# Kernel tuning notes

Hardware: AMD Instinct MI355X
Metric: run time of the kernel (lower is better)

## Reference

```python
import jax, jax.numpy as jnp
import numpy as np

N = 200000      # nodes
E = 1600000     # directed edges (before self-loops)
G = 5000        # graphs (molecules)
IN, HID, OUT, HEADS = 128, 128, 128, 3


def gat_layer(x, src, dst, W, a_src, a_dst, b, heads, out_dim, concat):
    n = x.shape[0]
    h = (x @ W).reshape(n, heads, out_dim)                 # [N,H,F]
    al_s = jnp.einsum('nhf,hf->nh', h, a_src)              # [N,H]
    al_d = jnp.einsum('nhf,hf->nh', h, a_dst)
    e = jax.nn.leaky_relu(al_s[src] + al_d[dst], 0.2)      # [E,H]
    m = jax.ops.segment_max(e, dst, num_segments=n)        # softmax over incoming edges
    ex = jnp.exp(e - m[dst])
    den = jax.ops.segment_sum(ex, dst, num_segments=n)
    alpha = ex / (den[dst] + 1e-16)                        # [E,H]
    msg = h[src] * alpha[..., None]                        # [E,H,F]
    agg = jax.ops.segment_sum(msg, dst, num_segments=n)    # [N,H,F]
    agg = agg.reshape(n, heads * out_dim) if concat else agg.mean(axis=1)
    return agg + b


def setup_inputs() -> dict:
    key = jax.random.key(0)
    ks = jax.random.split(key, 16)
    d = {}
    d['x'] = jax.random.normal(ks[0], (N, IN), dtype=jnp.float32)
    d['edge_index'] = jax.random.randint(ks[1], (2, E), 0, N, dtype=jnp.int64)
    d['batch'] = jnp.sort(jax.random.randint(ks[2], (N,), 0, G, dtype=jnp.int64))
    s = 0.1
    d['W1'] = jax.random.normal(ks[3], (IN, HEADS * HID), jnp.float32) * s
    d['a1s'] = jax.random.normal(ks[4], (HEADS, HID), jnp.float32) * s
    d['a1d'] = jax.random.normal(ks[5], (HEADS, HID), jnp.float32) * s
    d['b1'] = jnp.zeros((HEADS * HID,), jnp.float32)
    d['W2'] = jax.random.normal(ks[6], (HEADS * HID, HEADS * HID), jnp.float32) * s
    d['a2s'] = jax.random.normal(ks[7], (HEADS, HID), jnp.float32) * s
    d['a2d'] = jax.random.normal(ks[8], (HEADS, HID), jnp.float32) * s
    d['b2'] = jnp.zeros((HEADS * HID,), jnp.float32)
    d['W3'] = jax.random.normal(ks[9], (HEADS * HID, OUT), jnp.float32) * s
    d['a3s'] = jax.random.normal(ks[10], (1, OUT), jnp.float32) * s
    d['a3d'] = jax.random.normal(ks[11], (1, OUT), jnp.float32) * s
    d['b3'] = jnp.zeros((OUT,), jnp.float32)
    return d


def reference(x, edge_index, batch, W1, a1s, a1d, b1, W2, a2s, a2d, b2, W3, a3s, a3d, b3):
    # PyG GATConv default add_self_loops=True
    loops = jnp.arange(N, dtype=edge_index.dtype)
    src = jnp.concatenate([edge_index[0], loops])
    dst = jnp.concatenate([edge_index[1], loops])
    h = jax.nn.leaky_relu(gat_layer(x, src, dst, W1, a1s, a1d, b1, HEADS, HID, True), 0.2)
    h = jax.nn.leaky_relu(gat_layer(h, src, dst, W2, a2s, a2d, b2, HEADS, HID, True), 0.2)
    h = jax.nn.leaky_relu(gat_layer(h, src, dst, W3, a3s, a3d, b3, 1, OUT, False), 0.2)
    # global mean pool over graphs
    sums = jax.ops.segment_sum(h, batch, num_segments=G)            # [G,OUT]
    cnt = jax.ops.segment_sum(jnp.ones((N,), h.dtype), batch, num_segments=G)
    return sums / jnp.maximum(cnt, 1.0)[:, None]
```

## Files before the change

kernel.cpp:

```cpp
#include <hip/hip_runtime.h>
#include <hip/hip_bf16.h>
#include <math.h>

#define LRELU_SLOPE 0.2f
typedef __hip_bfloat16 bf16;
typedef __hip_bfloat162 bf16x2;

typedef short s8v __attribute__((ext_vector_type(8)));
typedef short s4v __attribute__((ext_vector_type(4)));
typedef float f4v __attribute__((ext_vector_type(4)));
typedef int   i4v __attribute__((ext_vector_type(4)));
typedef unsigned int u4v __attribute__((ext_vector_type(4)));

__device__ __forceinline__ float lrelu(float v) { return v > 0.f ? v : LRELU_SLOPE * v; }
__device__ __forceinline__ float b2f(short b) {
  return __uint_as_float(((unsigned)(unsigned short)b) << 16);
}

__device__ __forceinline__ void st2(float* p, float x, float y) {
  *(float2*)p = float2{x, y};
}

__device__ __forceinline__ u4v make_srd(const void* p) {
  u4v r;
  unsigned long long a = (unsigned long long)p;
  r.x = (unsigned)a; r.y = (unsigned)(a >> 32);
  r.z = 0xFFFFFFFFu;
  r.w = 0x00020000u;
  return r;
}
__device__ __forceinline__ void bstore16_nt(u4v srd, int byteoff, i4v d) {
  asm volatile("buffer_store_dwordx4 %0, %1, %2, 0 offen sc1 nt"
               :: "v"(d), "v"(byteoff), "s"(srd));
}


__global__ void k_zero(unsigned int* __restrict__ p, long n) {
  long i = (long)blockIdx.x * blockDim.x + threadIdx.x;
  if (i < n) p[i] = 0u;
}

__global__ void k_zero_out(float* __restrict__ out, int n) {
  int i = blockIdx.x * blockDim.x + threadIdx.x;
  if (i < n) out[i] = 0.f;
}


__global__ void k_cvt(const float* __restrict__ x, bf16* __restrict__ xb, long n8) {
  long i = (long)blockIdx.x * blockDim.x + threadIdx.x;
  if (i >= n8) return;
  const float4* xp = (const float4*)(x + i * 8);
  float4 a = xp[0], b = xp[1];
  s8v v;
  bf16 t;
  t = __float2bfloat16(a.x); v[0] = *(short*)&t;
  t = __float2bfloat16(a.y); v[1] = *(short*)&t;
  t = __float2bfloat16(a.z); v[2] = *(short*)&t;
  t = __float2bfloat16(a.w); v[3] = *(short*)&t;
  t = __float2bfloat16(b.x); v[4] = *(short*)&t;
  t = __float2bfloat16(b.y); v[5] = *(short*)&t;
  t = __float2bfloat16(b.z); v[6] = *(short*)&t;
  t = __float2bfloat16(b.w); v[7] = *(short*)&t;
  *(s8v*)&xb[i * 8] = v;
}

__global__ void k_tw2(const float* __restrict__ W, bf16* __restrict__ B2, int K, int NN) {
  int tid = blockIdx.x * blockDim.x + threadIdx.x;
  int total = (K * NN) >> 3;
  if (tid >= total) return;
  int f = tid >> 6, l = tid & 63;
  int nfr = NN >> 4;
  int k32 = f / nfr, ct = f - k32 * nfr;
  int col = ct * 16 + (l & 15);
  int krow = k32 * 32 + (l >> 4) * 8;
  s8v v;
#pragma unroll
  for (int j = 0; j < 8; ++j) {
    bf16 b = __float2bfloat16(W[(size_t)(krow + j) * NN + col]);
    v[j] = *(short*)&b;
  }
  *(s8v*)&B2[(size_t)tid * 8] = v;
}


__global__ void k_hist(const int* __restrict__ dst, int* __restrict__ deg, int E, int Et) {
  int e = blockIdx.x * blockDim.x + threadIdx.x;
  if (e >= Et) return;
  int d = (e < E) ? dst[e] : (e - E);
  atomicAdd(&deg[d], 1);
}

__global__ void k_hist1(const int* __restrict__ idx, int* __restrict__ deg, int n) {
  int i = blockIdx.x * blockDim.x + threadIdx.x;
  if (i < n) atomicAdd(&deg[idx[i]], 1);
}

__global__ void k_scan1(const int* __restrict__ deg, int* __restrict__ offs,
                        int* __restrict__ bsum, int n) {
  __shared__ int sd[256];
  int t = threadIdx.x;
  int base = blockIdx.x * 1024 + t * 4;
  int v[4]; int tsum = 0;
#pragma unroll
  for (int i = 0; i < 4; ++i) { v[i] = (base + i < n) ? deg[base + i] : 0; tsum += v[i]; }
  sd[t] = tsum;
  __syncthreads();
  for (int off = 1; off < 256; off <<= 1) {
    int x = (t >= off) ? sd[t - off] : 0;
    __syncthreads();
    sd[t] += x;
    __syncthreads();
  }
  int excl = sd[t] - tsum;
#pragma unroll
  for (int i = 0; i < 4; ++i) { if (base + i < n) offs[base + i] = excl; excl += v[i]; }
  if (t == 255) bsum[blockIdx.x] = sd[255];
}

__global__ void k_scan2(int* bsum, int nb) {
  int t = threadIdx.x;
  if (nb > 256) {
    if (t == 0 && blockIdx.x == 0) {
      int run = 0;
      for (int i = 0; i < nb; ++i) { int x = bsum[i]; bsum[i] = run; run += x; }
    }
    return;
  }
  int v = (t < nb) ? bsum[t] : 0;
  int lane = t & 63, wv = t >> 6;
  int s = v;
#pragma unroll
  for (int off = 1; off < 64; off <<= 1) {
    int u = __shfl_up(s, off, 64);
    if (lane >= off) s += u;
  }
  __shared__ int wsum[4];
  if (lane == 63) wsum[wv] = s;
  __syncthreads();
  int add = 0;
  for (int w = 0; w < wv; ++w) add += wsum[w];
  if (t < nb) bsum[t] = add + s - v;
}

__global__ void k_scan3(int* __restrict__ offs, const int* __restrict__ bsum, int n, int total) {
  int t = threadIdx.x;
  int base = blockIdx.x * 1024 + t * 4;
  int add = bsum[blockIdx.x];
#pragma unroll
  for (int i = 0; i < 4; ++i) if (base + i < n) offs[base + i] += add;
  if (blockIdx.x == 0 && t == 0) offs[n] = total;
}

__global__ void k_scatter(const int* __restrict__ src, const int* __restrict__ dst,
                          const int* __restrict__ offs, int* __restrict__ cur,
                          int* __restrict__ ssrc, int E, int Et) {
  int e = blockIdx.x * blockDim.x + threadIdx.x;
  if (e >= Et) return;
  int s, d;
  if (e < E) { s = src[e]; d = dst[e]; } else { s = d = e - E; }
  int pos = offs[d] + atomicAdd(&cur[d], 1);
  ssrc[pos] = s;
}


template <int K, int NN>
__global__ __launch_bounds__(512, 4) void k_gemm_t(const bf16* __restrict__ A,
                                                   const bf16* __restrict__ B2,
                                                   bf16* __restrict__ C,
                                                   const float* __restrict__ as_,
                                                   const float* __restrict__ ad_,
                                                   float* __restrict__ al_s,
                                                   float* __restrict__ al_d,
                                                   int N) {
  constexpr int nk = K / 32;
  constexpr int nfr = NN >> 4;
  constexpr int SP = (NN == 384) ? 4 : 1;
  __shared__ __align__(16) short sA[2][256 * 32];
  int t = threadIdx.x;
  int wv = t >> 6, lane = t & 63;
  int mg = wv >> 1, ng = wv & 1;
  int quad = lane >> 4, l15 = lane & 15;
  size_t bm0 = (size_t)blockIdx.x * 256;
  int hd = (NN == 384) ? blockIdx.y : 0;
  int ctb = blockIdx.y * 8 + ng * 4;

  int sr = t >> 2, p = t & 3;
  int c = p ^ (sr & 3);
  const bf16* g0 = A + (bm0 + sr) * (size_t)K + c * 8;
  const bf16* g1 = g0 + (size_t)128 * K;
  const bf16* Bp = B2 + ((size_t)ctb << 9) + lane * 8;

  f4v acc[4][4];
#pragma unroll
  for (int ms = 0; ms < 4; ++ms)
#pragma unroll
    for (int bn = 0; bn < 4; ++bn) acc[ms][bn] = f4v{0, 0, 0, 0};

#define STAGE(step, buf)                                                        \
  do {                                                                          \
    __builtin_amdgcn_global_load_lds(                                           \
        (const __attribute__((address_space(1))) void*)(g0 + (step) * 32),      \
        (__attribute__((address_space(3))) void*)((char*)sA[buf] + wv * 1024),  \
        16, 0, 0);                                                              \
    __builtin_amdgcn_global_load_lds(                                           \
        (const __attribute__((address_space(1))) void*)(g1 + (step) * 32),      \
        (__attribute__((address_space(3))) void*)((char*)sA[buf] + 8192 + wv * 1024), \
        16, 0, 0);                                                              \
  } while (0)

  STAGE(0, 0);
  __syncthreads();

  for (int ik = 0; ik < nk; ++ik) {
    int cur = ik & 1;
    if (ik + 1 < nk) STAGE(ik + 1, cur ^ 1);

    const char* sb = (const char*)sA[cur];
    s8v af[4];
#pragma unroll
    for (int ms = 0; ms < 4; ++ms) {
      int row = mg * 64 + ms * 16 + l15;
      int pos = quad ^ (row & 3);
      af[ms] = *(const s8v*)(sb + row * 64 + pos * 16);
    }
    s8v pb[4];
#pragma unroll
    for (int bn = 0; bn < 4; ++bn)
      pb[bn] = *(const s8v*)(Bp + ((size_t)(ik * nfr + bn) << 9));
#pragma unroll
    for (int ms = 0; ms < 4; ++ms)
#pragma unroll
      for (int bn = 0; bn < 4; ++bn)
        acc[ms][bn] = __builtin_amdgcn_mfma_f32_16x16x32_bf16(af[ms], pb[bn], acc[ms][bn], 0, 0, 0);

    __syncthreads();
  }
#undef STAGE

  float asv[4], adv[4];
#pragma unroll
  for (int bn = 0; bn < 4; ++bn) {
    int cwh = (ng * 4 + bn) * 16 + l15;
    asv[bn] = as_[hd * 128 + cwh];
    adv[bn] = ad_[hd * 128 + cwh];
  }

#pragma unroll
  for (int ms = 0; ms < 4; ++ms) {
#pragma unroll
    for (int r = 0; r < 4; ++r) {
      size_t rown = bm0 + mg * 64 + ms * 16 + quad * 4 + r;
      float ps = 0.f, pd = 0.f;
#pragma unroll
      for (int bn = 0; bn < 4; ++bn) {
        int coln = (ctb + bn) * 16 + l15;
        bf16 b = __float2bfloat16(acc[ms][bn][r]);
        C[rown * NN + coln] = b;
        float hv = b2f(*(short*)&b);
        ps += hv * asv[bn];
        pd += hv * adv[bn];
      }
#pragma unroll
      for (int off = 1; off <= 8; off <<= 1) {
        ps += __shfl_xor(ps, off, 64);
        pd += __shfl_xor(pd, off, 64);
      }
      if (l15 == 0 && rown < (size_t)N) {
        atomicAdd(&al_s[rown * SP + hd], ps);
        atomicAdd(&al_d[rown * SP + hd], pd);
      }
    }
  }
}


template <int CPL> struct HVec;
template <> struct HVec<8> { typedef s8v T; };
template <> struct HVec<4> { typedef s4v T; };

template <int H, typename OT>
__global__ __launch_bounds__(256) void k_attn_agg(const bf16* __restrict__ hbuf,
                           const int* __restrict__ ssrc,
                           const int* __restrict__ offs, const float* __restrict__ al_s,
                           const float* __restrict__ al_d, const float* __restrict__ bias,
                           OT* __restrict__ out, int N) {
  constexpr int SW  = (H > 1) ? 4 : 2;
  constexpr int ROW = H * 128;
  constexpr int CPL = (H > 1) ? 8 : 4;
  constexpr int NL  = ROW / CPL;
  typedef typename HVec<CPL>::T hvec;

  __shared__ __align__(16) float stash[4][64 * SW];
  int n = (blockIdx.x * blockDim.x + threadIdx.x) >> 6;
  int lane = threadIdx.x & 63;
  if (n >= N) return;
  float* st = stash[threadIdx.x >> 6];
  int start = offs[n], end = offs[n + 1];

  float ald[H];
  if constexpr (H > 1) {
    float4 t = *(const float4*)&al_d[(size_t)n * 4];
    ald[0] = t.x; ald[1] = t.y; ald[2] = t.z;
  } else {
    ald[0] = al_d[n];
  }

  bool act = lane < NL;
  int c0 = act ? lane * CPL : 0;
  int hd_l = c0 >> 7;

  float m[H];
  float den = 0.f;
  float acc[CPL];
#pragma unroll
  for (int hd = 0; hd < H; ++hd) m[hd] = -1e30f;
#pragma unroll
  for (int i = 0; i < CPL; ++i) acc[i] = 0.f;

  for (int cb = start; cb < end; cb += 64) {
    int cl = end - cb; if (cl > 64) cl = 64;
    bool el = lane < cl;
    int mys = el ? ssrc[cb + lane] : 0;
    float ev[H];
    if constexpr (H > 1) {
      float4 av = *(const float4*)&al_s[(size_t)mys * 4];
      ev[0] = av.x; ev[1] = av.y; ev[2] = av.z;
    } else {
      ev[0] = al_s[mys];
    }
#pragma unroll
    for (int hd = 0; hd < H; ++hd)
      ev[hd] = el ? lrelu(ev[hd] + ald[hd]) : -1e30f;

    float nm[H];
#pragma unroll
    for (int hd = 0; hd < H; ++hd) {
      float v = ev[hd];
#pragma unroll
      for (int off = 32; off; off >>= 1) v = fmaxf(v, __shfl_xor(v, off, 64));
      nm[hd] = fmaxf(v, m[hd]);
    }
    if (cb > start) {
      float sc[H];
#pragma unroll
      for (int hd = 0; hd < H; ++hd) sc[hd] = __expf(m[hd] - nm[hd]);
      float so = sc[hd_l];
      den *= so;
#pragma unroll
      for (int i = 0; i < CPL; ++i) acc[i] *= so;
    }
#pragma unroll
    for (int hd = 0; hd < H; ++hd) m[hd] = nm[hd];

    float myex[H];
#pragma unroll
    for (int hd = 0; hd < H; ++hd) myex[hd] = el ? __expf(ev[hd] - m[hd]) : 0.f;

    __builtin_amdgcn_wave_barrier();
    if constexpr (H > 1) {
      float4 s4{__int_as_float(mys), myex[0], myex[1], myex[2]};
      *(float4*)&st[lane * 4] = s4;
    } else {
      float2 s2{__int_as_float(mys), myex[0]};
      *(float2*)&st[lane * 2] = s2;
    }
    asm volatile("s_waitcnt lgkmcnt(0)" ::: "memory");
    __builtin_amdgcn_wave_barrier();

    for (int r = 0; r < cl; r += 8) {
      int su[8]; float a[8];
#pragma unroll
      for (int u = 0; u < 8; ++u) {
        if constexpr (H > 1) {
          float4 ed = *(const float4*)&st[(r + u) * 4];
          su[u] = __float_as_int(ed.x);
          a[u] = (hd_l == 0) ? ed.y : ((hd_l == 1) ? ed.z : ed.w);
        } else {
          float2 ed = *(const float2*)&st[(r + u) * 2];
          su[u] = __float_as_int(ed.x);
          a[u] = ed.y;
        }
        den += a[u];
      }
      hvec hv[8];
#pragma unroll
      for (int u = 0; u < 8; ++u)
        hv[u] = *(const hvec*)(hbuf + (size_t)su[u] * ROW + c0);
#pragma unroll
      for (int u = 0; u < 8; ++u)
#pragma unroll
        for (int i = 0; i < CPL; ++i)
          acc[i] += a[u] * b2f(hv[u][i]);
    }
  }

  if (act) {
    float rr = 1.f / (den + 1e-16f);
    u4v srd = make_srd(out);
    int boff = (int)(((size_t)n * ROW + c0) * sizeof(OT));
    if constexpr (sizeof(OT) == 2) {
      union { s8v s; i4v i; } u;
#pragma unroll
      for (int i = 0; i < CPL; ++i) {
        float o = lrelu(acc[i] * rr + bias[c0 + i]);
        bf16 b = __float2bfloat16(o);
        u.s[i] = *(short*)&b;
      }
      bstore16_nt(srd, boff, u.i);
    } else {
      union { float4 f; i4v i; } u;
      u.f.x = lrelu(acc[0] * rr + bias[c0 + 0]);
      u.f.y = lrelu(acc[1] * rr + bias[c0 + 1]);
      u.f.z = lrelu(acc[2] * rr + bias[c0 + 2]);
      u.f.w = lrelu(acc[3] * rr + bias[c0 + 3]);
      bstore16_nt(srd, boff, u.i);
    }
  }
}


__global__ void k_pool(const float* __restrict__ h, const int* __restrict__ goffs,
                       float* __restrict__ out, int G) {
  int g = (blockIdx.x * blockDim.x + threadIdx.x) >> 6;
  int lane = threadIdx.x & 63;
  if (g >= G) return;
  int s = goffs[g], e = goffs[g + 1];
  float ax = 0.f, ay = 0.f;
  for (int n = s; n < e; ++n) {
    float2 v = *(const float2*)&h[(size_t)n * 128 + lane * 2];
    ax += v.x; ay += v.y;
  }
  float c = fmaxf((float)(e - s), 1.f);
  st2(&out[(size_t)g * 128 + lane * 2], ax / c, ay / c);
}


extern "C" void kernel_launch(void* const* d_in, const int* in_sizes, int n_in,
                              void* d_out, int out_size, void* d_ws, size_t ws_size,
                              hipStream_t stream) {
  const float* x   = (const float*)d_in[0];
  const int*   ei  = (const int*)d_in[1];
  const int*   bat = (const int*)d_in[2];
  const float* W1  = (const float*)d_in[3];
  const float* a1s = (const float*)d_in[4];
  const float* a1d = (const float*)d_in[5];
  const float* b1  = (const float*)d_in[6];
  const float* W2  = (const float*)d_in[7];
  const float* a2s = (const float*)d_in[8];
  const float* a2d = (const float*)d_in[9];
  const float* b2  = (const float*)d_in[10];
  const float* W3  = (const float*)d_in[11];
  const float* a3s = (const float*)d_in[12];
  const float* a3d = (const float*)d_in[13];
  const float* b3  = (const float*)d_in[14];
  float* out = (float*)d_out;

  const int N = in_sizes[2];
  const int E = in_sizes[1] / 2;
  const int Et = E + N;
  const int G = out_size / 128;

  const int MB = (N + 255) / 256;
  const int Mpad = MB * 256;

  char* p = (char*)d_ws;
  auto carve = [&](size_t bytes) { void* r = (void*)p; p += (bytes + 255) & ~(size_t)255; return r; };
  bf16*  bufA   = (bf16*)carve((size_t)Mpad * 384 * 2);
  bf16*  bufB   = (bf16*)carve((size_t)Mpad * 384 * 2);
  float* al_s   = (float*)carve((size_t)N * 4 * 4);
  float* al_d   = (float*)carve((size_t)N * 4 * 4);
  int*   ssrc   = (int*)carve((size_t)Et * 4);
  int*   offs   = (int*)carve((size_t)(N + 1) * 4);
  int*   deg    = (int*)carve((size_t)N * 4);
  int*   cur    = (int*)carve((size_t)N * 4);
  int*   bsum   = (int*)carve(4096 * 4);
  int*   gdeg   = (int*)carve((size_t)G * 4);
  int*   goffs  = (int*)carve((size_t)(G + 1) * 4);
  bf16*  Wp1    = (bf16*)carve((size_t)384 * 128 * 2);
  bf16*  Wp2    = (bf16*)carve((size_t)384 * 384 * 2);
  bf16*  Wp3    = (bf16*)carve((size_t)128 * 384 * 2);
  size_t need = (size_t)(p - (char*)d_ws);

  if (ws_size < need) {
    k_zero_out<<<(out_size + 255) / 256, 256, 0, stream>>>(out, out_size);
    return;
  }

  const int* esrc = ei;
  const int* edst = ei + E;

  int ebl = (Et + 255) / 256;
  int NB = (N + 1023) / 1024;
  int GB = (G + 1023) / 1024;
  int nodeWaveBlocks = (N * 64 + 255) / 256;
  long alWords = (long)N * 8;
  int alBlocks = (int)((alWords + 255) / 256);

  bf16* xb = bufA;
  k_cvt<<<((long)N * 128 / 8 + 255) / 256, 256, 0, stream>>>(x, xb, (long)N * 128 / 8);
  k_tw2<<<(128 * 384 / 8 + 255) / 256, 256, 0, stream>>>(W1, Wp1, 128, 384);
  k_tw2<<<(384 * 384 / 8 + 255) / 256, 256, 0, stream>>>(W2, Wp2, 384, 384);
  k_tw2<<<(384 * 128 / 8 + 255) / 256, 256, 0, stream>>>(W3, Wp3, 384, 128);

  k_zero<<<(N + 255) / 256, 256, 0, stream>>>((unsigned int*)deg, N);
  k_hist<<<ebl, 256, 0, stream>>>(edst, deg, E, Et);
  k_scan1<<<NB, 256, 0, stream>>>(deg, offs, bsum, N);
  k_scan2<<<1, 256, 0, stream>>>(bsum, NB);
  k_scan3<<<NB, 256, 0, stream>>>(offs, bsum, N, Et);
  k_zero<<<(N + 255) / 256, 256, 0, stream>>>((unsigned int*)cur, N);
  k_scatter<<<ebl, 256, 0, stream>>>(esrc, edst, offs, cur, ssrc, E, Et);

  k_zero<<<(G + 255) / 256, 256, 0, stream>>>((unsigned int*)gdeg, G);
  k_hist1<<<(N + 255) / 256, 256, 0, stream>>>(bat, gdeg, N);
  k_scan1<<<GB, 256, 0, stream>>>(gdeg, goffs, bsum, G);
  k_scan2<<<1, 256, 0, stream>>>(bsum, GB);
  k_scan3<<<GB, 256, 0, stream>>>(goffs, bsum, G, N);

  k_zero<<<alBlocks, 256, 0, stream>>>((unsigned int*)al_s, alWords);
  k_gemm_t<128, 384><<<dim3(MB, 3), 512, 0, stream>>>(xb, Wp1, bufB, a1s, a1d, al_s, al_d, N);
  k_attn_agg<3, bf16><<<nodeWaveBlocks, 256, 0, stream>>>(bufB, ssrc, offs, al_s, al_d, b1, bufA, N);

  k_zero<<<alBlocks, 256, 0, stream>>>((unsigned int*)al_s, alWords);
  k_gemm_t<384, 384><<<dim3(MB, 3), 512, 0, stream>>>(bufA, Wp2, bufB, a2s, a2d, al_s, al_d, N);
  k_attn_agg<3, bf16><<<nodeWaveBlocks, 256, 0, stream>>>(bufB, ssrc, offs, al_s, al_d, b2, bufA, N);

  k_zero<<<alBlocks, 256, 0, stream>>>((unsigned int*)al_s, alWords);
  k_gemm_t<384, 128><<<dim3(MB, 1), 512, 0, stream>>>(bufA, Wp3, bufB, a3s, a3d, al_s, al_d, N);
  float* out3 = (float*)bufA;
  k_attn_agg<1, float><<<nodeWaveBlocks, 256, 0, stream>>>(bufB, ssrc, offs, al_s, al_d, b3, out3, N);

  k_pool<<<(G * 64 + 255) / 256, 256, 0, stream>>>(out3, goffs, out, G);
}
```

Measured before the change: 1.474 ms.

## Stage GEMM epilogue through LDS for coalesced stores and drop attention atomics

The GEMM epilogue now writes bf16 results into a padded LDS tile, then stores full 16-byte rows to global memory. The per-row attention logits are computed from those rows and written directly instead of through atomicAdd, so the zeroing kernels for the logit buffers are removed. The grid is flattened so the head index is the fastest-varying part of the block id, which places blocks that read the same A rows next to each other for cache reuse. The LDS swizzle gains an extra XOR term to cut bank conflicts. In exchange the epilogue adds two extra barriers and LDS round trips.

```diff
diff --git a/kernel.cpp b/kernel.cpp
--- a/kernel.cpp
+++ b/kernel.cpp
@@ -163,7 +163,7 @@
 }
 
 
-template <int K, int NN>
+template <int K, int NN, int NY, int SP>
 __global__ __launch_bounds__(512, 4) void k_gemm_t(const bf16* __restrict__ A,
                                                    const bf16* __restrict__ B2,
                                                    bf16* __restrict__ C,
@@ -174,21 +174,24 @@
                                                    int N) {
   constexpr int nk = K / 32;
   constexpr int nfr = NN >> 4;
-  constexpr int SP = (NN == 384) ? 4 : 1;
-  __shared__ __align__(16) short sA[2][256 * 32];
+  __shared__ __align__(16) char smem[34816];
   int t = threadIdx.x;
   int wv = t >> 6, lane = t & 63;
   int mg = wv >> 1, ng = wv & 1;
   int quad = lane >> 4, l15 = lane & 15;
-  size_t bm0 = (size_t)blockIdx.x * 256;
-  int hd = (NN == 384) ? blockIdx.y : 0;
-  int ctb = blockIdx.y * 8 + ng * 4;
+  int bid = blockIdx.x;
+  int hd = bid % NY;
+  size_t bm0 = (size_t)(bid / NY) * 256;
+  int ctb = hd * 8 + ng * 4;
+  int coff = hd * 128;
 
   int sr = t >> 2, p = t & 3;
-  int c = p ^ (sr & 3);
+  int c = p ^ (sr & 3) ^ ((sr >> 2) & 3);
   const bf16* g0 = A + (bm0 + sr) * (size_t)K + c * 8;
   const bf16* g1 = g0 + (size_t)128 * K;
   const bf16* Bp = B2 + ((size_t)ctb << 9) + lane * 8;
+  char* sA0 = smem;
+  char* sA1 = smem + 16384;
 
   f4v acc[4][4];
 #pragma unroll
@@ -196,31 +199,31 @@
 #pragma unroll
     for (int bn = 0; bn < 4; ++bn) acc[ms][bn] = f4v{0, 0, 0, 0};
 
-#define STAGE(step, buf)                                                        \
+#define STAGE(step, bufp)                                                       \
   do {                                                                          \
     __builtin_amdgcn_global_load_lds(                                           \
         (const __attribute__((address_space(1))) void*)(g0 + (step) * 32),      \
-        (__attribute__((address_space(3))) void*)((char*)sA[buf] + wv * 1024),  \
+        (__attribute__((address_space(3))) void*)((bufp) + wv * 1024),          \
         16, 0, 0);                                                              \
     __builtin_amdgcn_global_load_lds(                                           \
         (const __attribute__((address_space(1))) void*)(g1 + (step) * 32),      \
-        (__attribute__((address_space(3))) void*)((char*)sA[buf] + 8192 + wv * 1024), \
+        (__attribute__((address_space(3))) void*)((bufp) + 8192 + wv * 1024),   \
         16, 0, 0);                                                              \
   } while (0)
 
-  STAGE(0, 0);
+  STAGE(0, sA0);
   __syncthreads();
 
   for (int ik = 0; ik < nk; ++ik) {
     int cur = ik & 1;
-    if (ik + 1 < nk) STAGE(ik + 1, cur ^ 1);
-
-    const char* sb = (const char*)sA[cur];
+    if (ik + 1 < nk) STAGE(ik + 1, cur ? sA0 : sA1);
+
+    const char* sb = cur ? sA1 : sA0;
     s8v af[4];
 #pragma unroll
     for (int ms = 0; ms < 4; ++ms) {
       int row = mg * 64 + ms * 16 + l15;
-      int pos = quad ^ (row & 3);
+      int pos = quad ^ (row & 3) ^ ((row >> 2) & 3);
       af[ms] = *(const s8v*)(sb + row * 64 + pos * 16);
     }
     s8v pb[4];
@@ -237,39 +240,53 @@
   }
 #undef STAGE
 
-  float asv[4], adv[4];
-#pragma unroll
-  for (int bn = 0; bn < 4; ++bn) {
-    int cwh = (ng * 4 + bn) * 16 + l15;
-    asv[bn] = as_[hd * 128 + cwh];
-    adv[bn] = ad_[hd * 128 + cwh];
-  }
-
-#pragma unroll
-  for (int ms = 0; ms < 4; ++ms) {
-#pragma unroll
-    for (int r = 0; r < 4; ++r) {
-      size_t rown = bm0 + mg * 64 + ms * 16 + quad * 4 + r;
-      float ps = 0.f, pd = 0.f;
-#pragma unroll
-      for (int bn = 0; bn < 4; ++bn) {
-        int coln = (ctb + bn) * 16 + l15;
-        bf16 b = __float2bfloat16(acc[ms][bn][r]);
-        C[rown * NN + coln] = b;
-        float hv = b2f(*(short*)&b);
-        ps += hv * asv[bn];
-        pd += hv * adv[bn];
-      }
+  short* stg = (short*)smem;
+  const float* asb = as_ + coff;
+  const float* adb = ad_ + coff;
+#pragma unroll
+  for (int ph = 0; ph < 2; ++ph) {
+    if ((mg >> 1) == ph) {
+      int rbase = (mg & 1) * 64;
+#pragma unroll
+      for (int ms = 0; ms < 4; ++ms)
+#pragma unroll
+        for (int bn = 0; bn < 4; ++bn) {
+          int cl = (ng * 4 + bn) * 16 + l15;
+#pragma unroll
+          for (int r = 0; r < 4; ++r) {
+            int rl = rbase + ms * 16 + quad * 4 + r;
+            bf16 b = __float2bfloat16(acc[ms][bn][r]);
+            stg[rl * 136 + cl] = *(short*)&b;
+          }
+        }
+    }
+    __syncthreads();
+#pragma unroll
+    for (int k2 = 0; k2 < 4; ++k2) {
+      int cid = k2 * 512 + t;
+      int row = cid >> 4, ch = cid & 15;
+      s8v v = *(const s8v*)&stg[row * 136 + ch * 8];
+      size_t rowg = bm0 + ph * 128 + row;
+      *(s8v*)&C[rowg * NN + coff + ch * 8] = v;
+      float4 a0 = *(const float4*)(asb + ch * 8);
+      float4 a1 = *(const float4*)(asb + ch * 8 + 4);
+      float4 d0 = *(const float4*)(adb + ch * 8);
+      float4 d1 = *(const float4*)(adb + ch * 8 + 4);
+      float ps = b2f(v[0]) * a0.x + b2f(v[1]) * a0.y + b2f(v[2]) * a0.z + b2f(v[3]) * a0.w
+               + b2f(v[4]) * a1.x + b2f(v[5]) * a1.y + b2f(v[6]) * a1.z + b2f(v[7]) * a1.w;
+      float pd = b2f(v[0]) * d0.x + b2f(v[1]) * d0.y + b2f(v[2]) * d0.z + b2f(v[3]) * d0.w
+               + b2f(v[4]) * d1.x + b2f(v[5]) * d1.y + b2f(v[6]) * d1.z + b2f(v[7]) * d1.w;
 #pragma unroll
       for (int off = 1; off <= 8; off <<= 1) {
         ps += __shfl_xor(ps, off, 64);
         pd += __shfl_xor(pd, off, 64);
       }
-      if (l15 == 0 && rown < (size_t)N) {
-        atomicAdd(&al_s[rown * SP + hd], ps);
-        atomicAdd(&al_d[rown * SP + hd], pd);
+      if (ch == 0 && rowg < (size_t)N) {
+        al_s[rowg * SP + hd] = ps;
+        al_d[rowg * SP + hd] = pd;
       }
     }
+    __syncthreads();
   }
 }
 
@@ -493,8 +510,6 @@
   int NB = (N + 1023) / 1024;
   int GB = (G + 1023) / 1024;
   int nodeWaveBlocks = (N * 64 + 255) / 256;
-  long alWords = (long)N * 8;
-  int alBlocks = (int)((alWords + 255) / 256);
 
   bf16* xb = bufA;
   k_cvt<<<((long)N * 128 / 8 + 255) / 256, 256, 0, stream>>>(x, xb, (long)N * 128 / 8);
@@ -516,16 +531,13 @@
   k_scan2<<<1, 256, 0, stream>>>(bsum, GB);
   k_scan3<<<GB, 256, 0, stream>>>(goffs, bsum, G, N);
 
-  k_zero<<<alBlocks, 256, 0, stream>>>((unsigned int*)al_s, alWords);
-  k_gemm_t<128, 384><<<dim3(MB, 3), 512, 0, stream>>>(xb, Wp1, bufB, a1s, a1d, al_s, al_d, N);
+  k_gemm_t<128, 384, 3, 4><<<MB * 3, 512, 0, stream>>>(xb, Wp1, bufB, a1s, a1d, al_s, al_d, N);
   k_attn_agg<3, bf16><<<nodeWaveBlocks, 256, 0, stream>>>(bufB, ssrc, offs, al_s, al_d, b1, bufA, N);
 
-  k_zero<<<alBlocks, 256, 0, stream>>>((unsigned int*)al_s, alWords);
-  k_gemm_t<384, 384><<<dim3(MB, 3), 512, 0, stream>>>(bufA, Wp2, bufB, a2s, a2d, al_s, al_d, N);
+  k_gemm_t<384, 384, 3, 4><<<MB * 3, 512, 0, stream>>>(bufA, Wp2, bufB, a2s, a2d, al_s, al_d, N);
   k_attn_agg<3, bf16><<<nodeWaveBlocks, 256, 0, stream>>>(bufB, ssrc, offs, al_s, al_d, b2, bufA, N);
 
-  k_zero<<<alBlocks, 256, 0, stream>>>((unsigned int*)al_s, alWords);
-  k_gemm_t<384, 128><<<dim3(MB, 1), 512, 0, stream>>>(bufA, Wp3, bufB, a3s, a3d, al_s, al_d, N);
+  k_gemm_t<384, 128, 1, 1><<<MB, 512, 0, stream>>>(bufA, Wp3, bufB, a3s, a3d, al_s, al_d, N);
   float* out3 = (float*)bufA;
   k_attn_agg<1, float><<<nodeWaveBlocks, 256, 0, stream>>>(bufB, ssrc, offs, al_s, al_d, b3, out3, N);
 
```

Measured after the change: 1.271 ms. 1.16x faster.
